# Kernel optimization log

Hardware: AMD Instinct MI355X
Metric: run time of the kernel (lower is better)

Reference implementation:

```python
import jax, jax.numpy as jnp
import numpy as np

B, N_IN, O, IN_L, OUT_L = 256, 1152, 10, 8, 16
ITERS = 3
EPS = 1e-7

def squash(s, eps):
    # norm over the capsule-length axis (-2), keepdim, as in the torch code
    dot = jnp.sum(s * s, axis=-2, keepdims=True)
    return (dot / (1.0 + dot) / jnp.sqrt(dot + eps)) * s

def setup_inputs() -> dict:
    key = jax.random.key(0)
    k1, k2, k3 = jax.random.split(key, 3)
    x = jax.random.normal(k1, (B, N_IN, IN_L, 1), dtype=jnp.float32)
    weight = 0.05 * jax.random.normal(k2, (1, N_IN, O, IN_L, OUT_L), dtype=jnp.float32)
    bias = 0.05 * jax.random.normal(k3, (1, 1, O, OUT_L, 1), dtype=jnp.float32)
    return {"x": x, "weight": weight, "bias": bias}

def reference(x, weight, bias):
    # u_hat[b,n,o,k] = sum_i W[0,n,o,i,k] * x[b,n,i,0]  -> (B, N, O, K, 1)
    u_hat = jnp.einsum('noik,bni->bnok', weight[0], x[..., 0])[..., None]
    u_det = jax.lax.stop_gradient(u_hat)
    b_ij = jnp.zeros((x.shape[0], N_IN, O, 1, 1), dtype=x.dtype)
    v = None
    for r in range(ITERS):
        c = jax.nn.softmax(b_ij, axis=2)          # routing coefficients over out caps
        u = u_hat if r == ITERS - 1 else u_det    # detached except last iter
        s = jnp.sum(c * u, axis=1, keepdims=True) + bias  # (B,1,O,K,1)
        v = squash(s, EPS)
        if r != ITERS - 1:
            # agreement: sum over capsule-length axis 3 -> (B,N,O,1,1)
            b_ij = b_ij + jnp.sum(u_det * v, axis=3, keepdims=True)
    return v
```

## Files before the change

### kernel.cpp

```cpp
#include <hip/hip_runtime.h>
#include <hip/hip_bf16.h>

#define BB   256
#define NIN  1152
#define OO   10
#define IL   8
#define OL   16
#define ROW  (OO*OL)
#define EPSQ 1e-7f
#define NT   8
#define BT   32

typedef unsigned short ushx8 __attribute__((ext_vector_type(8)));
typedef unsigned short ushx4 __attribute__((ext_vector_type(4)));

__device__ __forceinline__ float bf2f(unsigned short h) {
    unsigned u = ((unsigned)h) << 16;
    return __builtin_bit_cast(float, u);
}

__global__ __launch_bounds__(160) void caps_build(
    const float* __restrict__ x, const float* __restrict__ w,
    unsigned short* __restrict__ u)
{
    __shared__ float4 wl4[NT][321];
    __shared__ float4 xl4[BT * 16];
    const int t  = threadIdx.x;
    const int n0 = blockIdx.x * NT;
    const int b0 = blockIdx.y * BT;

    const float4* wg = reinterpret_cast<const float4*>(w) + (size_t)n0 * 320;
    for (int j = t; j < NT * 320; j += 160) {
        const int row = j / 320;
        const int lin = j - row * 320;
        const int o   = lin >> 5;
        const int rem = lin & 31;
        const int i   = rem >> 2;
        const int kh  = rem & 3;
        const int ip  = i ^ (o & 1);
        wl4[row][(o << 5) | (ip << 2) | kh] = wg[j];
    }
    const float4* xg = reinterpret_cast<const float4*>(x);
    for (int j = t; j < BT * 16; j += 160) {
        const int bl = j >> 4;
        const int r  = j & 15;
        xl4[j] = xg[((size_t)(b0 + bl) * NIN + n0) * 2 + r];
    }
    __syncthreads();

    const int nl = t / 20;
    const int s  = t - nl * 20;
    const int o  = s >> 1;
    const int k8 = s & 1;
    const int p  = o & 1;
    const float4* wbase = &wl4[nl][(o << 5) | (k8 << 1)];
    const float4* xbase = &xl4[nl * 2];
    unsigned short* ub = u + ((size_t)b0 * NIN + n0 + nl) * ROW + o * OL + k8 * 8;
    const size_t ustride = (size_t)NIN * ROW;

    for (int bl = 0; bl < BT; bl += 4) {
        float xv[4][IL];
        #pragma unroll
        for (int bb = 0; bb < 4; ++bb) {
            const float4 x0 = xbase[(bl + bb) * 16];
            const float4 x1 = xbase[(bl + bb) * 16 + 1];
            xv[bb][0] = x0.x; xv[bb][1] = x0.y; xv[bb][2] = x0.z; xv[bb][3] = x0.w;
            xv[bb][4] = x1.x; xv[bb][5] = x1.y; xv[bb][6] = x1.z; xv[bb][7] = x1.w;
        }

        float acc[4][8];
        #pragma unroll
        for (int bb = 0; bb < 4; ++bb)
            #pragma unroll
            for (int j = 0; j < 8; ++j) acc[bb][j] = 0.f;

        #pragma unroll
        for (int i = 0; i < IL; ++i) {
            const float4 wlo = wbase[(i ^ p) << 2];
            const float4 whi = wbase[((i ^ p) << 2) | 1];
            const float wv[8] = {wlo.x, wlo.y, wlo.z, wlo.w, whi.x, whi.y, whi.z, whi.w};
            #pragma unroll
            for (int bb = 0; bb < 4; ++bb)
                #pragma unroll
                for (int j = 0; j < 8; ++j)
                    acc[bb][j] = fmaf(wv[j], xv[bb][i], acc[bb][j]);
        }

        #pragma unroll
        for (int bb = 0; bb < 4; ++bb) {
            union { ushx8 v; __hip_bfloat162 h[4]; } pk;
            #pragma unroll
            for (int j = 0; j < 4; ++j)
                pk.h[j] = __float22bfloat162_rn(make_float2(acc[bb][2*j], acc[bb][2*j+1]));
            *reinterpret_cast<ushx8*>(ub + (size_t)(bl + bb) * ustride) = pk.v;
        }
    }
}

__global__ __launch_bounds__(768) void caps_route3(
    const unsigned short* __restrict__ u, const float* __restrict__ bias,
    float* __restrict__ outv)
{
    __shared__ float lds[12][ROW];
    __shared__ float vbuf[ROW];
    const int t  = threadIdx.x;
    const int q  = t & 3;
    const int g  = t >> 2;
    const int wv = t >> 6;
    const int b  = blockIdx.x;
    const unsigned short* ub = u + (size_t)b * NIN * ROW;

    float bsv = 0.f;
    if (t < ROW) bsv = bias[t];
    float vprev = 0.f;

    #pragma unroll
    for (int iter = 0; iter < 3; ++iter) {
        float sp[5][8];
        #pragma unroll
        for (int j = 0; j < 5; ++j)
            #pragma unroll
            for (int e = 0; e < 8; ++e) sp[j][e] = 0.f;

        if (iter == 0) {
            for (int m = 0; m < 6; ++m) {
                const unsigned short* un = ub + (size_t)(g + m * 192) * ROW;
                #pragma unroll
                for (int j = 0; j < 5; ++j) {
                    const ushx8 raw = *reinterpret_cast<const ushx8*>(un + (q + 4 * j) * 8);
                    #pragma unroll
                    for (int e = 0; e < 8; ++e) sp[j][e] += bf2f(raw[e]);
                }
            }
        } else {
            float vs[5][8];
            #pragma unroll
            for (int j = 0; j < 5; ++j) {
                #pragma unroll
                for (int e = 0; e < 8; ++e) vs[j][e] = vbuf[(q + 4 * j) * 8 + e];
            }

            for (int m = 0; m < 6; ++m) {
                const unsigned short* un = ub + (size_t)(g + m * 192) * ROW;
                float uf[5][8];
                #pragma unroll
                for (int j = 0; j < 5; ++j) {
                    const ushx8 raw = *reinterpret_cast<const ushx8*>(un + (q + 4 * j) * 8);
                    #pragma unroll
                    for (int e = 0; e < 8; ++e) uf[j][e] = bf2f(raw[e]);
                }

                float d[5], dd[5];
                #pragma unroll
                for (int j = 0; j < 5; ++j) {
                    float acc = uf[j][0] * vs[j][0];
                    #pragma unroll
                    for (int e = 1; e < 8; ++e) acc = fmaf(uf[j][e], vs[j][e], acc);
                    acc += __shfl_xor(acc, 1, 4);
                    d[j] = acc;
                }
                #pragma unroll
                for (int j = 0; j < 5; ++j) dd[j] = __shfl_xor(d[j], 2, 4);

                float mx = fmaxf(d[0], dd[0]);
                #pragma unroll
                for (int j = 1; j < 5; ++j) mx = fmaxf(mx, fmaxf(d[j], dd[j]));
                float se = 0.f, e_[5];
                #pragma unroll
                for (int j = 0; j < 5; ++j) {
                    e_[j] = __expf(d[j] - mx);
                    se += e_[j] + __expf(dd[j] - mx);
                }
                const float r = 1.f / se;
                #pragma unroll
                for (int j = 0; j < 5; ++j) {
                    const float c = e_[j] * r;
                    #pragma unroll
                    for (int e = 0; e < 8; ++e)
                        sp[j][e] = fmaf(c, uf[j][e], sp[j][e]);
                }
            }
        }

        #pragma unroll
        for (int j = 0; j < 5; ++j)
            #pragma unroll
            for (int e = 0; e < 8; ++e) {
                #pragma unroll
                for (int msk = 4; msk <= 32; msk <<= 1)
                    sp[j][e] += __shfl_xor(sp[j][e], msk);
            }
        if ((t & 63) < 4) {
            #pragma unroll
            for (int j = 0; j < 5; ++j)
                #pragma unroll
                for (int e = 0; e < 8; ++e)
                    lds[wv][(q + 4 * j) * 8 + e] = sp[j][e];
        }
        __syncthreads();

        if (t < ROW) {
            float ssum = 0.f;
            #pragma unroll
            for (int wvi = 0; wvi < 12; ++wvi) ssum += lds[wvi][t];
            const float sv = (iter == 0 ? 0.1f : 1.0f) * ssum + bsv;

            float dq = sv * sv;
            dq += __shfl_xor(dq, 1, 16);
            dq += __shfl_xor(dq, 2, 16);
            dq += __shfl_xor(dq, 4, 16);
            dq += __shfl_xor(dq, 8, 16);
            const float f = dq / ((1.f + dq) * sqrtf(dq + EPSQ));
            const float v = f * sv;

            if (iter == 0) { vbuf[t] = v; vprev = v; }
            else if (iter == 1) { vbuf[t] = v + vprev; }
            else { outv[(size_t)b * ROW + t] = v; }
        }
        __syncthreads();
    }
}

extern "C" void kernel_launch(void* const* d_in, const int* in_sizes, int n_in,
                              void* d_out, int out_size, void* d_ws, size_t ws_size,
                              hipStream_t stream) {
    const float* x    = (const float*)d_in[0];
    const float* w    = (const float*)d_in[1];
    const float* bias = (const float*)d_in[2];
    float* out = (float*)d_out;

    unsigned short* u = (unsigned short*)d_ws;

    caps_build<<<dim3(NIN / NT, BB / BT), 160, 0, stream>>>(x, w, u);
    caps_route3<<<BB, 768, 0, stream>>>(u, bias, out);
}
```

Before: 85.56 us.

## Halve build tile per block and software-prefetch u rows in routing loop

The build kernel now handles 4 input capsules per block instead of 8, splitting the 32-batch tile across two thread halves of 16 batches each. This doubles the grid and halves shared memory per block to raise occupancy. The routing kernel fully unrolls its 6-step loop and double-buffers the bf16 row loads, issuing the next row's global loads before computing on the current one to hide memory latency. The cost is higher register pressure at 768 threads per block, which could cause spills.

```diff
diff --git a/kernel.cpp b/kernel.cpp
--- a/kernel.cpp
+++ b/kernel.cpp
@@ -8,11 +8,10 @@
 #define OL   16
 #define ROW  (OO*OL)
 #define EPSQ 1e-7f
-#define NT   8
+#define NT   4
 #define BT   32
 
 typedef unsigned short ushx8 __attribute__((ext_vector_type(8)));
-typedef unsigned short ushx4 __attribute__((ext_vector_type(4)));
 
 __device__ __forceinline__ float bf2f(unsigned short h) {
     unsigned u = ((unsigned)h) << 16;
@@ -24,46 +23,52 @@
     unsigned short* __restrict__ u)
 {
     __shared__ float4 wl4[NT][321];
-    __shared__ float4 xl4[BT * 16];
+    __shared__ float4 xl4[BT * 8];
     const int t  = threadIdx.x;
     const int n0 = blockIdx.x * NT;
     const int b0 = blockIdx.y * BT;
 
     const float4* wg = reinterpret_cast<const float4*>(w) + (size_t)n0 * 320;
-    for (int j = t; j < NT * 320; j += 160) {
+    #pragma unroll
+    for (int jj = 0; jj < 8; ++jj) {
+        const int j   = t + jj * 160;
         const int row = j / 320;
         const int lin = j - row * 320;
         const int o   = lin >> 5;
         const int rem = lin & 31;
         const int i   = rem >> 2;
         const int kh  = rem & 3;
-        const int ip  = i ^ (o & 1);
-        wl4[row][(o << 5) | (ip << 2) | kh] = wg[j];
+        wl4[row][(o << 5) | ((i ^ (o & 1)) << 2) | kh] = wg[j];
     }
     const float4* xg = reinterpret_cast<const float4*>(x);
-    for (int j = t; j < BT * 16; j += 160) {
-        const int bl = j >> 4;
-        const int r  = j & 15;
-        xl4[j] = xg[((size_t)(b0 + bl) * NIN + n0) * 2 + r];
+    {
+        int j = t;
+        xl4[j] = xg[((size_t)(b0 + (j >> 3)) * NIN + n0) * 2 + (j & 7)];
+        j = t + 160;
+        if (j < BT * 8)
+            xl4[j] = xg[((size_t)(b0 + (j >> 3)) * NIN + n0) * 2 + (j & 7)];
     }
     __syncthreads();
 
-    const int nl = t / 20;
-    const int s  = t - nl * 20;
+    const int nl = t / 40;
+    const int r  = t - nl * 40;
+    const int hh = r / 20;
+    const int s  = r - hh * 20;
     const int o  = s >> 1;
     const int k8 = s & 1;
     const int p  = o & 1;
     const float4* wbase = &wl4[nl][(o << 5) | (k8 << 1)];
-    const float4* xbase = &xl4[nl * 2];
-    unsigned short* ub = u + ((size_t)b0 * NIN + n0 + nl) * ROW + o * OL + k8 * 8;
+    const float4* xbase = &xl4[(hh * 16) * 8 + nl * 2];
+    unsigned short* ub = u + ((size_t)(b0 + hh * 16) * NIN + n0 + nl) * ROW
+                           + o * OL + k8 * 8;
     const size_t ustride = (size_t)NIN * ROW;
 
-    for (int bl = 0; bl < BT; bl += 4) {
+    for (int bl = 0; bl < 16; bl += 4) {
         float xv[4][IL];
         #pragma unroll
         for (int bb = 0; bb < 4; ++bb) {
-            const float4 x0 = xbase[(bl + bb) * 16];
-            const float4 x1 = xbase[(bl + bb) * 16 + 1];
+            const float4 x0 = xbase[(bl + bb) * 8];
+            const float4 x1 = xbase[(bl + bb) * 8 + 1];
             xv[bb][0] = x0.x; xv[bb][1] = x0.y; xv[bb][2] = x0.z; xv[bb][3] = x0.w;
             xv[bb][4] = x1.x; xv[bb][5] = x1.y; xv[bb][6] = x1.z; xv[bb][7] = x1.w;
         }
@@ -122,14 +127,30 @@
             #pragma unroll
             for (int e = 0; e < 8; ++e) sp[j][e] = 0.f;
 
+        ushx8 raw[5], nxt[5];
+        {
+            const unsigned short* un0 = ub + (size_t)g * ROW;
+            #pragma unroll
+            for (int j = 0; j < 5; ++j)
+                raw[j] = *reinterpret_cast<const ushx8*>(un0 + (q + 4 * j) * 8);
+        }
+
         if (iter == 0) {
+            #pragma unroll
             for (int m = 0; m < 6; ++m) {
-                const unsigned short* un = ub + (size_t)(g + m * 192) * ROW;
-                #pragma unroll
-                for (int j = 0; j < 5; ++j) {
-                    const ushx8 raw = *reinterpret_cast<const ushx8*>(un + (q + 4 * j) * 8);
-                    #pragma unroll
-                    for (int e = 0; e < 8; ++e) sp[j][e] += bf2f(raw[e]);
+                if (m < 5) {
+                    const unsigned short* un = ub + (size_t)(g + (m + 1) * 192) * ROW;
+                    #pragma unroll
+                    for (int j = 0; j < 5; ++j)
+                        nxt[j] = *reinterpret_cast<const ushx8*>(un + (q + 4 * j) * 8);
+                }
+                #pragma unroll
+                for (int j = 0; j < 5; ++j)
+                    #pragma unroll
+                    for (int e = 0; e < 8; ++e) sp[j][e] += bf2f(raw[j][e]);
+                if (m < 5) {
+                    #pragma unroll
+                    for (int j = 0; j < 5; ++j) raw[j] = nxt[j];
                 }
             }
         } else {
@@ -140,15 +161,20 @@
                 for (int e = 0; e < 8; ++e) vs[j][e] = vbuf[(q + 4 * j) * 8 + e];
             }
 
+            #pragma unroll
             for (int m = 0; m < 6; ++m) {
-                const unsigned short* un = ub + (size_t)(g + m * 192) * ROW;
+                if (m < 5) {
+                    const unsigned short* un = ub + (size_t)(g + (m + 1) * 192) * ROW;
+                    #pragma unroll
+                    for (int j = 0; j < 5; ++j)
+                        nxt[j] = *reinterpret_cast<const ushx8*>(un + (q + 4 * j) * 8);
+                }
+
                 float uf[5][8];
                 #pragma unroll
-                for (int j = 0; j < 5; ++j) {
-                    const ushx8 raw = *reinterpret_cast<const ushx8*>(un + (q + 4 * j) * 8);
-                    #pragma unroll
-                    for (int e = 0; e < 8; ++e) uf[j][e] = bf2f(raw[e]);
-                }
+                for (int j = 0; j < 5; ++j)
+                    #pragma unroll
+                    for (int e = 0; e < 8; ++e) uf[j][e] = bf2f(raw[j][e]);
 
                 float d[5], dd[5];
                 #pragma unroll
@@ -171,13 +197,18 @@
                     e_[j] = __expf(d[j] - mx);
                     se += e_[j] + __expf(dd[j] - mx);
                 }
-                const float r = 1.f / se;
+                const float rinv = 1.f / se;
                 #pragma unroll
                 for (int j = 0; j < 5; ++j) {
-                    const float c = e_[j] * r;
+                    const float c = e_[j] * rinv;
                     #pragma unroll
                     for (int e = 0; e < 8; ++e)
                         sp[j][e] = fmaf(c, uf[j][e], sp[j][e]);
+                }
+
+                if (m < 5) {
+                    #pragma unroll
+                    for (int j = 0; j < 5; ++j) raw[j] = nxt[j];
                 }
             }
         }
```

After: 181.1 us. +111.7%, slower.

## Fuse first routing iteration's sum into u_hat build via fp32 partial sums

Applied to the files above, without the earlier changes.

The build kernel now also accumulates per-chunk fp32 partial sums of u_hat over input capsules. A small new kernel reduces these partials and applies squash to get v0, so the routing kernel skips the first full pass over the bf16 u buffer and runs only two iterations. The build kernel is also restructured: each thread now handles one batch row across 32 input capsules, staging weights in LDS in 4-capsule sub-tiles, instead of covering several batch rows per weight tile. This adds a third launch and a partial-sum workspace, and changes the tiling and weight reuse of the build stage.

```diff
diff --git a/kernel.cpp b/kernel.cpp
--- a/kernel.cpp
+++ b/kernel.cpp
@@ -8,98 +8,128 @@
 #define OL   16
 #define ROW  (OO*OL)
 #define EPSQ 1e-7f
-#define NT   8
-#define BT   32
+#define NTT  32
+#define BT2  16
+#define NCH2 (NIN/NTT)
 
 typedef unsigned short ushx8 __attribute__((ext_vector_type(8)));
-typedef unsigned short ushx4 __attribute__((ext_vector_type(4)));
 
 __device__ __forceinline__ float bf2f(unsigned short h) {
     unsigned u = ((unsigned)h) << 16;
     return __builtin_bit_cast(float, u);
 }
 
-__global__ __launch_bounds__(160) void caps_build(
+__global__ __launch_bounds__(320) void caps_build2(
     const float* __restrict__ x, const float* __restrict__ w,
-    unsigned short* __restrict__ u)
+    unsigned short* __restrict__ u, float* __restrict__ psum)
 {
-    __shared__ float4 wl4[NT][321];
-    __shared__ float4 xl4[BT * 16];
-    const int t  = threadIdx.x;
-    const int n0 = blockIdx.x * NT;
-    const int b0 = blockIdx.y * BT;
-
-    const float4* wg = reinterpret_cast<const float4*>(w) + (size_t)n0 * 320;
-    for (int j = t; j < NT * 320; j += 160) {
-        const int row = j / 320;
-        const int lin = j - row * 320;
-        const int o   = lin >> 5;
-        const int rem = lin & 31;
-        const int i   = rem >> 2;
-        const int kh  = rem & 3;
-        const int ip  = i ^ (o & 1);
-        wl4[row][(o << 5) | (ip << 2) | kh] = wg[j];
-    }
-    const float4* xg = reinterpret_cast<const float4*>(x);
-    for (int j = t; j < BT * 16; j += 160) {
-        const int bl = j >> 4;
-        const int r  = j & 15;
-        xl4[j] = xg[((size_t)(b0 + bl) * NIN + n0) * 2 + r];
-    }
-    __syncthreads();
-
-    const int nl = t / 20;
-    const int s  = t - nl * 20;
-    const int o  = s >> 1;
-    const int k8 = s & 1;
-    const int p  = o & 1;
-    const float4* wbase = &wl4[nl][(o << 5) | (k8 << 1)];
-    const float4* xbase = &xl4[nl * 2];
-    unsigned short* ub = u + ((size_t)b0 * NIN + n0 + nl) * ROW + o * OL + k8 * 8;
-    const size_t ustride = (size_t)NIN * ROW;
-
-    for (int bl = 0; bl < BT; bl += 4) {
-        float xv[4][IL];
-        #pragma unroll
-        for (int bb = 0; bb < 4; ++bb) {
-            const float4 x0 = xbase[(bl + bb) * 16];
-            const float4 x1 = xbase[(bl + bb) * 16 + 1];
-            xv[bb][0] = x0.x; xv[bb][1] = x0.y; xv[bb][2] = x0.z; xv[bb][3] = x0.w;
-            xv[bb][4] = x1.x; xv[bb][5] = x1.y; xv[bb][6] = x1.z; xv[bb][7] = x1.w;
-        }
-
-        float acc[4][8];
-        #pragma unroll
-        for (int bb = 0; bb < 4; ++bb)
-            #pragma unroll
-            for (int j = 0; j < 8; ++j) acc[bb][j] = 0.f;
-
-        #pragma unroll
-        for (int i = 0; i < IL; ++i) {
-            const float4 wlo = wbase[(i ^ p) << 2];
-            const float4 whi = wbase[((i ^ p) << 2) | 1];
-            const float wv[8] = {wlo.x, wlo.y, wlo.z, wlo.w, whi.x, whi.y, whi.z, whi.w};
-            #pragma unroll
-            for (int bb = 0; bb < 4; ++bb)
-                #pragma unroll
-                for (int j = 0; j < 8; ++j)
-                    acc[bb][j] = fmaf(wv[j], xv[bb][i], acc[bb][j]);
-        }
-
-        #pragma unroll
-        for (int bb = 0; bb < 4; ++bb) {
+    __shared__ float4 wl4[4][321];
+    const int t    = threadIdx.x;
+    const int bloc = t / 20;
+    const int oct  = t - bloc * 20;
+    const int o    = oct >> 1;
+    const int k8   = oct & 1;
+    const int p    = o & 1;
+    const int n0   = blockIdx.x * NTT;
+    const int b    = blockIdx.y * BT2 + bloc;
+
+    const float* xb = x + ((size_t)b * NIN + n0) * 8;
+    unsigned short* ub = u + ((size_t)b * NIN + n0) * ROW + o * OL + k8 * 8;
+
+    float ps[8];
+    #pragma unroll
+    for (int j = 0; j < 8; ++j) ps[j] = 0.f;
+
+    for (int sub = 0; sub < 8; ++sub) {
+        __syncthreads();
+        const float4* wg = reinterpret_cast<const float4*>(w)
+                         + (size_t)(n0 + sub * 4) * 320;
+        #pragma unroll
+        for (int jj = 0; jj < 4; ++jj) {
+            const int j   = t + jj * 320;
+            const int row = j / 320;
+            const int lin = j - row * 320;
+            const int o2  = lin >> 5;
+            const int rem = lin & 31;
+            const int i2  = rem >> 2;
+            const int kh  = rem & 3;
+            wl4[row][(o2 << 5) | ((i2 ^ (o2 & 1)) << 2) | kh] = wg[j];
+        }
+        __syncthreads();
+
+        #pragma unroll
+        for (int nn = 0; nn < 4; ++nn) {
+            const int nrel = sub * 4 + nn;
+            const float4 x0 = *reinterpret_cast<const float4*>(xb + nrel * 8);
+            const float4 x1 = *reinterpret_cast<const float4*>(xb + nrel * 8 + 4);
+            const float xv[IL] = {x0.x, x0.y, x0.z, x0.w, x1.x, x1.y, x1.z, x1.w};
+
+            float acc[8];
+            #pragma unroll
+            for (int j = 0; j < 8; ++j) acc[j] = 0.f;
+
+            const float4* wbase = &wl4[nn][(o << 5) | (k8 << 1)];
+            #pragma unroll
+            for (int i = 0; i < IL; ++i) {
+                const float4 wlo = wbase[(i ^ p) << 2];
+                const float4 whi = wbase[((i ^ p) << 2) | 1];
+                acc[0] = fmaf(wlo.x, xv[i], acc[0]);
+                acc[1] = fmaf(wlo.y, xv[i], acc[1]);
+                acc[2] = fmaf(wlo.z, xv[i], acc[2]);
+                acc[3] = fmaf(wlo.w, xv[i], acc[3]);
+                acc[4] = fmaf(whi.x, xv[i], acc[4]);
+                acc[5] = fmaf(whi.y, xv[i], acc[5]);
+                acc[6] = fmaf(whi.z, xv[i], acc[6]);
+                acc[7] = fmaf(whi.w, xv[i], acc[7]);
+            }
+
             union { ushx8 v; __hip_bfloat162 h[4]; } pk;
             #pragma unroll
             for (int j = 0; j < 4; ++j)
-                pk.h[j] = __float22bfloat162_rn(make_float2(acc[bb][2*j], acc[bb][2*j+1]));
-            *reinterpret_cast<ushx8*>(ub + (size_t)(bl + bb) * ustride) = pk.v;
-        }
-    }
-}
-
-__global__ __launch_bounds__(768) void caps_route3(
+                pk.h[j] = __float22bfloat162_rn(make_float2(acc[2*j], acc[2*j+1]));
+            *reinterpret_cast<ushx8*>(ub + (size_t)nrel * ROW) = pk.v;
+
+            #pragma unroll
+            for (int j = 0; j < 8; ++j) ps[j] += acc[j];
+        }
+    }
+
+    float* pp = psum + ((size_t)blockIdx.x * BB + b) * ROW + oct * 8;
+    *reinterpret_cast<float4*>(pp)     = make_float4(ps[0], ps[1], ps[2], ps[3]);
+    *reinterpret_cast<float4*>(pp + 4) = make_float4(ps[4], ps[5], ps[6], ps[7]);
+}
+
+__global__ __launch_bounds__(192) void caps_squash0(
+    const float* __restrict__ psum, const float* __restrict__ bias,
+    float* __restrict__ v0)
+{
+    const int t = threadIdx.x;
+    if (t >= ROW) return;
+    const int b = blockIdx.x;
+
+    float s0 = 0.f, s1 = 0.f, s2 = 0.f, s3 = 0.f;
+    const float* pt = psum + (size_t)b * ROW + t;
+    #pragma unroll
+    for (int ch = 0; ch < NCH2; ch += 4) {
+        s0 += pt[(size_t)(ch + 0) * BB * ROW];
+        s1 += pt[(size_t)(ch + 1) * BB * ROW];
+        s2 += pt[(size_t)(ch + 2) * BB * ROW];
+        s3 += pt[(size_t)(ch + 3) * BB * ROW];
+    }
+    const float s = 0.1f * ((s0 + s1) + (s2 + s3)) + bias[t];
+
+    float d = s * s;
+    d += __shfl_xor(d, 1, 16);
+    d += __shfl_xor(d, 2, 16);
+    d += __shfl_xor(d, 4, 16);
+    d += __shfl_xor(d, 8, 16);
+    const float f = d / ((1.f + d) * sqrtf(d + EPSQ));
+    v0[(size_t)b * ROW + t] = f * s;
+}
+
+__global__ __launch_bounds__(768) void caps_route2(
     const unsigned short* __restrict__ u, const float* __restrict__ bias,
-    float* __restrict__ outv)
+    const float* __restrict__ v0g, float* __restrict__ outv)
 {
     __shared__ float lds[12][ROW];
     __shared__ float vbuf[ROW];
@@ -111,74 +141,68 @@
     const unsigned short* ub = u + (size_t)b * NIN * ROW;
 
     float bsv = 0.f;
-    if (t < ROW) bsv = bias[t];
     float vprev = 0.f;
+    if (t < ROW) {
+        bsv = bias[t];
+        const float v = v0g[(size_t)b * ROW + t];
+        vbuf[t] = v;
+        vprev = v;
+    }
+    __syncthreads();
 
     #pragma unroll
-    for (int iter = 0; iter < 3; ++iter) {
+    for (int iter = 1; iter < 3; ++iter) {
         float sp[5][8];
         #pragma unroll
         for (int j = 0; j < 5; ++j)
             #pragma unroll
             for (int e = 0; e < 8; ++e) sp[j][e] = 0.f;
 
-        if (iter == 0) {
-            for (int m = 0; m < 6; ++m) {
-                const unsigned short* un = ub + (size_t)(g + m * 192) * ROW;
-                #pragma unroll
-                for (int j = 0; j < 5; ++j) {
-                    const ushx8 raw = *reinterpret_cast<const ushx8*>(un + (q + 4 * j) * 8);
-                    #pragma unroll
-                    for (int e = 0; e < 8; ++e) sp[j][e] += bf2f(raw[e]);
-                }
-            }
-        } else {
-            float vs[5][8];
-            #pragma unroll
-            for (int j = 0; j < 5; ++j) {
-                #pragma unroll
-                for (int e = 0; e < 8; ++e) vs[j][e] = vbuf[(q + 4 * j) * 8 + e];
-            }
-
-            for (int m = 0; m < 6; ++m) {
-                const unsigned short* un = ub + (size_t)(g + m * 192) * ROW;
-                float uf[5][8];
-                #pragma unroll
-                for (int j = 0; j < 5; ++j) {
-                    const ushx8 raw = *reinterpret_cast<const ushx8*>(un + (q + 4 * j) * 8);
-                    #pragma unroll
-                    for (int e = 0; e < 8; ++e) uf[j][e] = bf2f(raw[e]);
-                }
-
-                float d[5], dd[5];
-                #pragma unroll
-                for (int j = 0; j < 5; ++j) {
-                    float acc = uf[j][0] * vs[j][0];
-                    #pragma unroll
-                    for (int e = 1; e < 8; ++e) acc = fmaf(uf[j][e], vs[j][e], acc);
-                    acc += __shfl_xor(acc, 1, 4);
-                    d[j] = acc;
-                }
-                #pragma unroll
-                for (int j = 0; j < 5; ++j) dd[j] = __shfl_xor(d[j], 2, 4);
-
-                float mx = fmaxf(d[0], dd[0]);
-                #pragma unroll
-                for (int j = 1; j < 5; ++j) mx = fmaxf(mx, fmaxf(d[j], dd[j]));
-                float se = 0.f, e_[5];
-                #pragma unroll
-                for (int j = 0; j < 5; ++j) {
-                    e_[j] = __expf(d[j] - mx);
-                    se += e_[j] + __expf(dd[j] - mx);
-                }
-                const float r = 1.f / se;
-                #pragma unroll
-                for (int j = 0; j < 5; ++j) {
-                    const float c = e_[j] * r;
-                    #pragma unroll
-                    for (int e = 0; e < 8; ++e)
-                        sp[j][e] = fmaf(c, uf[j][e], sp[j][e]);
-                }
+        float vs[5][8];
+        #pragma unroll
+        for (int j = 0; j < 5; ++j) {
+            #pragma unroll
+            for (int e = 0; e < 8; ++e) vs[j][e] = vbuf[(q + 4 * j) * 8 + e];
+        }
+
+        for (int m = 0; m < 6; ++m) {
+            const unsigned short* un = ub + (size_t)(g + m * 192) * ROW;
+            float uf[5][8];
+            #pragma unroll
+            for (int j = 0; j < 5; ++j) {
+                const ushx8 raw = *reinterpret_cast<const ushx8*>(un + (q + 4 * j) * 8);
+                #pragma unroll
+                for (int e = 0; e < 8; ++e) uf[j][e] = bf2f(raw[e]);
+            }
+
+            float d[5], dd[5];
+            #pragma unroll
+            for (int j = 0; j < 5; ++j) {
+                float acc = uf[j][0] * vs[j][0];
+                #pragma unroll
+                for (int e = 1; e < 8; ++e) acc = fmaf(uf[j][e], vs[j][e], acc);
+                acc += __shfl_xor(acc, 1, 4);
+                d[j] = acc;
+            }
+            #pragma unroll
+            for (int j = 0; j < 5; ++j) dd[j] = __shfl_xor(d[j], 2, 4);
+
+            float mx = fmaxf(d[0], dd[0]);
+            #pragma unroll
+            for (int j = 1; j < 5; ++j) mx = fmaxf(mx, fmaxf(d[j], dd[j]));
+            float se = 0.f, e_[5];
+            #pragma unroll
+            for (int j = 0; j < 5; ++j) {
+                e_[j] = __expf(d[j] - mx);
+                se += e_[j] + __expf(dd[j] - mx);
+            }
+            const float r = 1.f / se;
+            #pragma unroll
+            for (int j = 0; j < 5; ++j) {
+                const float c = e_[j] * r;
+                #pragma unroll
+                for (int e = 0; e < 8; ++e)
+                    sp[j][e] = fmaf(c, uf[j][e], sp[j][e]);
             }
         }
 
@@ -203,7 +227,7 @@
             float ssum = 0.f;
             #pragma unroll
             for (int wvi = 0; wvi < 12; ++wvi) ssum += lds[wvi][t];
-            const float sv = (iter == 0 ? 0.1f : 1.0f) * ssum + bsv;
+            const float sv = ssum + bsv;
 
             float dq = sv * sv;
             dq += __shfl_xor(dq, 1, 16);
@@ -213,9 +237,8 @@
             const float f = dq / ((1.f + dq) * sqrtf(dq + EPSQ));
             const float v = f * sv;
 
-            if (iter == 0) { vbuf[t] = v; vprev = v; }
-            else if (iter == 1) { vbuf[t] = v + vprev; }
-            else { outv[(size_t)b * ROW + t] = v; }
+            if (iter == 1) { vbuf[t] = v + vprev; }
+            else           { outv[(size_t)b * ROW + t] = v; }
         }
         __syncthreads();
     }
@@ -230,7 +253,10 @@
     float* out = (float*)d_out;
 
     unsigned short* u = (unsigned short*)d_ws;
-
-    caps_build<<<dim3(NIN / NT, BB / BT), 160, 0, stream>>>(x, w, u);
-    caps_route3<<<BB, 768, 0, stream>>>(u, bias, out);
-}
+    float* psum = (float*)((char*)d_ws + (size_t)BB * NIN * ROW * 2);
+    float* v0   = psum + (size_t)NCH2 * BB * ROW;
+
+    caps_build2<<<dim3(NIN / NTT, BB / BT2), 320, 0, stream>>>(x, w, u, psum);
+    caps_squash0<<<BB, 192, 0, stream>>>(psum, bias, v0);
+    caps_route2<<<BB, 768, 0, stream>>>(u, bias, v0, out);
+}
```

Measured after the change: 95.21 us. 1.11x slower.
